# Performance work log

Measured on AMD Instinct MI355X. Metric: run time of the kernel, lower is better.

The kernel has to match this reference:

```python
import jax, jax.numpy as jnp
import numpy as np

N = 100000   # nodes in batched graph
E = 1600000  # edges (before self-loops)
D = 128      # in_dim == hidden_dim == num_outputs
G = 64       # graphs in the batch


def setup_inputs() -> dict:
    key = jax.random.key(0)
    ks = jax.random.split(key, 8)
    s = 1.0 / np.sqrt(D)
    x = jax.random.normal(ks[0], (N, D), jnp.float32)
    src = jax.random.randint(ks[1], (E,), 0, N, dtype=jnp.int64)
    dst = jax.random.randint(ks[2], (E,), 0, N, dtype=jnp.int64)
    graph_ids = jnp.sort(jax.random.randint(ks[3], (N,), 0, G, dtype=jnp.int64))
    W0 = jax.random.normal(ks[4], (D, D), jnp.float32) * s
    W1 = jax.random.normal(ks[5], (D, D), jnp.float32) * s
    W2 = jax.random.normal(ks[6], (D, D), jnp.float32) * s
    b0 = jnp.zeros((D,), jnp.float32)
    b1 = jnp.zeros((D,), jnp.float32)
    b2 = jnp.zeros((D,), jnp.float32)
    return {"x": x, "W0": W0, "b0": b0, "W1": W1, "b1": b1,
            "W2": W2, "b2": b2, "src": src, "dst": dst, "graph_ids": graph_ids}


def reference(x, W0, b0, W1, b1, W2, b2, src, dst, graph_ids):
    n = x.shape[0]
    loops = jnp.arange(n, dtype=src.dtype)
    src_f = jnp.concatenate([src, loops])  # add self-loops once (dgl.add_self_loop)
    dst_f = jnp.concatenate([dst, loops])
    ones_e = jnp.ones(src_f.shape, x.dtype)
    deg_out = jax.ops.segment_sum(ones_e, src_f, num_segments=n)  # >=1 (self-loop)
    deg_in = jax.ops.segment_sum(ones_e, dst_f, num_segments=n)
    cs = jax.lax.rsqrt(deg_out)[:, None]  # source norm (GraphConv norm='both')
    cd = jax.lax.rsqrt(deg_in)[:, None]   # destination norm

    def gcn_layer(h, W, b):
        m = (h * cs)[src_f]                                   # [E+N, D] gather
        agg = jax.ops.segment_sum(m, dst_f, num_segments=n)   # scatter-add SpMM
        return jax.nn.relu((agg * cd) @ W + b)                # F.relu(conv(g, h))

    h = gcn_layer(x, W0, b0)
    h = gcn_layer(h, W1, b1)
    h = gcn_layer(h, W2, b2)

    # dgl.mean_nodes: per-graph mean over nodes
    sums = jax.ops.segment_sum(h, graph_ids, num_segments=G)
    cnt = jax.ops.segment_sum(jnp.ones((n, 1), h.dtype), graph_ids, num_segments=G)
    return sums / jnp.maximum(cnt, 1.0)  # [G, D] logits
```

## Files before the change

### kernel.cpp

```cpp
#include <hip/hip_runtime.h>
#include <stdint.h>

#define D 128
#define CAP 64
#define HB 128
#define CH 25000

typedef __attribute__((ext_vector_type(8))) short bf16x8;
typedef __attribute__((ext_vector_type(4))) float f32x4;

__device__ inline unsigned short f2bf(float x) {
  union { float f; uint32_t u; } v; v.f = x;
  uint32_t u = v.u;
  u += 0x7fffu + ((u >> 16) & 1u);
  return (unsigned short)(u >> 16);
}
__device__ inline float bflo(uint32_t u) {
  union { uint32_t u; float f; } v; v.u = u << 16; return v.f;
}
__device__ inline float bfhi(uint32_t u) {
  union { uint32_t u; float f; } v; v.u = u & 0xffff0000u; return v.f;
}
__device__ inline uint32_t packbf(float lo, float hi) {
  return (uint32_t)f2bf(lo) | ((uint32_t)f2bf(hi) << 16);
}

__global__ __launch_bounds__(256) void hist_kernel(
    const int* __restrict__ src, const int* __restrict__ dst,
    unsigned int* __restrict__ parts_s, unsigned int* __restrict__ parts_d,
    int E, int N,
    const float* __restrict__ W0, const float* __restrict__ W1,
    const float* __restrict__ W2, unsigned short* __restrict__ Wt,
    int* __restrict__ cnt, int G, float* __restrict__ outz, int out_total) {
  __shared__ unsigned int lbs[CH / 8];
  __shared__ unsigned int lbd[CH / 8];
  int b = blockIdx.x & (HB - 1);
  int lo = (blockIdx.x >> 7) * CH;
  for (int i = threadIdx.x; i < CH / 8; i += 256) { lbs[i] = 0; lbd[i] = 0; }
  __syncthreads();
  int per = (E + HB - 1) / HB;
  int e0 = b * per;
  int e1 = min(e0 + per, E);
  for (int e = e0 + threadIdx.x; e < e1; e += 256) {
    int rs = src[e] - lo;
    if ((unsigned)rs < CH) atomicAdd(&lbs[rs >> 3], 1u << ((rs & 7) * 4));
    int rd = dst[e] - lo;
    if ((unsigned)rd < CH) atomicAdd(&lbd[rd >> 3], 1u << ((rd & 7) * 4));
  }
  __syncthreads();
  int nu = (N + 7) / 8;
  int base = lo >> 3;
  int cu = min(CH / 8, nu - base);
  unsigned int* ps = parts_s + (size_t)b * nu + base;
  unsigned int* pd = parts_d + (size_t)b * nu + base;
  for (int i = threadIdx.x; i < cu; i += 256) { ps[i] = lbs[i]; pd[i] = lbd[i]; }

  int gs = gridDim.x * 256;
  for (int i = blockIdx.x * 256 + threadIdx.x; i < 3 * 16384; i += gs) {
    int l = i >> 14, r = i & 16383;
    int n = r >> 7, k = r & 127;
    const float* W = (l == 0) ? W0 : (l == 1) ? W1 : W2;
    Wt[i] = f2bf(W[k * 128 + n]);
  }
  for (int i = blockIdx.x * 256 + threadIdx.x; i < G; i += gs) cnt[i] = 0;
  for (int i = blockIdx.x * 256 + threadIdx.x; i < out_total; i += gs) outz[i] = 0.f;
}

__global__ __launch_bounds__(256) void scan_norm_kernel(
    const unsigned char* __restrict__ parts_s,
    const unsigned char* __restrict__ parts_d,
    unsigned char* __restrict__ offs_d,
    int* __restrict__ degd,
    float* __restrict__ cs, float* __restrict__ cd,
    const int* __restrict__ gid, int* __restrict__ cnt,
    int N, int G) {
  __shared__ int lcnt[256];
  for (int i = threadIdx.x; i < G; i += 256) lcnt[i] = 0;
  __syncthreads();

  int t = blockIdx.x * blockDim.x + threadIdx.x;
  int i0 = t * 2;
  if (i0 < N) {
    int nb = N / 2;
    int ds0 = 0, ds1 = 0, dd0 = 0, dd1 = 0;
    for (int b = 0; b < HB; b++) {
      unsigned char sv = parts_s[(size_t)b * nb + t];
      ds0 += sv & 15; ds1 += sv >> 4;
      unsigned char dv = parts_d[(size_t)b * nb + t];
      offs_d[(size_t)b * N + i0]     = (unsigned char)min(dd0, 255);
      offs_d[(size_t)b * N + i0 + 1] = (unsigned char)min(dd1, 255);
      dd0 += dv & 15; dd1 += dv >> 4;
    }
    degd[i0] = dd0;     degd[i0 + 1] = dd1;
    cs[i0] = rsqrtf((float)ds0 + 1.0f);
    cs[i0 + 1] = rsqrtf((float)ds1 + 1.0f);
    cd[i0] = rsqrtf((float)dd0 + 1.0f);
    cd[i0 + 1] = rsqrtf((float)dd1 + 1.0f);
    atomicAdd(&lcnt[gid[i0]], 1);
    if (i0 + 1 < N) atomicAdd(&lcnt[gid[i0 + 1]], 1);
  }
  __syncthreads();
  for (int i = threadIdx.x; i < G; i += 256) {
    int c = lcnt[i];
    if (c) atomicAdd(&cnt[i], c);
  }
}

__global__ __launch_bounds__(256) void fill_kernel(
    const int* __restrict__ src, const int* __restrict__ dst,
    const unsigned char* __restrict__ offs_d, int* __restrict__ col, int E, int N,
    const float* __restrict__ x, const float* __restrict__ cs,
    uint32_t* __restrict__ xs) {
  __shared__ unsigned int lcur[CH / 8];
  int b = blockIdx.x & (HB - 1);
  int lo = (blockIdx.x >> 7) * CH;
  for (int i = threadIdx.x; i < CH / 8; i += 256) lcur[i] = 0;
  __syncthreads();
  int per = (E + HB - 1) / HB;
  int e0 = b * per;
  int e1 = min(e0 + per, E);
  const unsigned char* offb = offs_d + (size_t)b * N;
  for (int e = e0 + threadIdx.x; e < e1; e += 256) {
    int d = dst[e];
    int rd = d - lo;
    if ((unsigned)rd < CH) {
      unsigned old = atomicAdd(&lcur[rd >> 3], 1u << ((rd & 7) * 4));
      int local = (old >> ((rd & 7) * 4)) & 0xF;
      int pos = (int)offb[d] + local;
      if (pos < CAP) col[(size_t)d * CAP + pos] = src[e];
    }
  }
  int total2 = N * 64;
  int gs = gridDim.x * 256;
  for (int i = blockIdx.x * 256 + threadIdx.x; i < total2; i += gs) {
    float2 v = ((const float2*)x)[i];
    float c = cs[i >> 6];
    xs[i] = packbf(v.x * c, v.y * c);
  }
}

__global__ __launch_bounds__(512) void fused_layer_kernel(
    const uint32_t* __restrict__ hin, const unsigned short* __restrict__ Wt,
    const float* __restrict__ bias, const float* __restrict__ cd,
    const float* __restrict__ rowscale, const int* __restrict__ degd,
    const int* __restrict__ col, unsigned short* __restrict__ hout, int N) {
  __shared__ __align__(16) uint32_t At[16 * 68];

  int wv = threadIdx.x >> 6;
  int lane = threadIdx.x & 63;
  int m = lane & 15;
  int quad = lane >> 4;

  bf16x8 bfr[4];
#pragma unroll
  for (int c = 0; c < 4; c++)
    bfr[c] = *(const bf16x8*)(Wt + (size_t)(16 * wv + m) * 128 + c * 32 + quad * 8);

#pragma unroll
  for (int j = 0; j < 2; j++) {
    int w = __builtin_amdgcn_readfirstlane(blockIdx.x * 16 + wv * 2 + j);
    float accx = 0.f, accy = 0.f;
    if (w < N) {
      int n = min(degd[w], CAP);
      const int* cw = col + (size_t)w * CAP;
      const uint32_t* hl = hin + lane;
      uint32_t selfv = hl[(size_t)w * 64];
      accx = bflo(selfv); accy = bfhi(selfv);
      int i = 0;
      for (; i + 7 < n; i += 8) {
        int s0 = cw[i],     s1 = cw[i + 1], s2 = cw[i + 2], s3 = cw[i + 3];
        int s4 = cw[i + 4], s5 = cw[i + 5], s6 = cw[i + 6], s7 = cw[i + 7];
        uint32_t v0 = hl[(size_t)s0 * 64];
        uint32_t v1 = hl[(size_t)s1 * 64];
        uint32_t v2 = hl[(size_t)s2 * 64];
        uint32_t v3 = hl[(size_t)s3 * 64];
        uint32_t v4 = hl[(size_t)s4 * 64];
        uint32_t v5 = hl[(size_t)s5 * 64];
        uint32_t v6 = hl[(size_t)s6 * 64];
        uint32_t v7 = hl[(size_t)s7 * 64];
        accx += bflo(v0); accy += bfhi(v0);
        accx += bflo(v1); accy += bfhi(v1);
        accx += bflo(v2); accy += bfhi(v2);
        accx += bflo(v3); accy += bfhi(v3);
        accx += bflo(v4); accy += bfhi(v4);
        accx += bflo(v5); accy += bfhi(v5);
        accx += bflo(v6); accy += bfhi(v6);
        accx += bflo(v7); accy += bfhi(v7);
      }
      for (; i + 3 < n; i += 4) {
        int s0 = cw[i], s1 = cw[i + 1], s2 = cw[i + 2], s3 = cw[i + 3];
        uint32_t v0 = hl[(size_t)s0 * 64];
        uint32_t v1 = hl[(size_t)s1 * 64];
        uint32_t v2 = hl[(size_t)s2 * 64];
        uint32_t v3 = hl[(size_t)s3 * 64];
        accx += bflo(v0); accy += bfhi(v0);
        accx += bflo(v1); accy += bfhi(v1);
        accx += bflo(v2); accy += bfhi(v2);
        accx += bflo(v3); accy += bfhi(v3);
      }
      for (; i < n; i++) {
        uint32_t v = hl[(size_t)cw[i] * 64];
        accx += bflo(v); accy += bfhi(v);
      }
      float cdv = cd[w];
      accx *= cdv; accy *= cdv;
    }
    At[(wv * 2 + j) * 68 + lane] = packbf(accx, accy);
  }
  __syncthreads();

  const unsigned short* arow = (const unsigned short*)At + m * 136;
  f32x4 acc = f32x4{0.f, 0.f, 0.f, 0.f};
#pragma unroll
  for (int c = 0; c < 4; c++) {
    bf16x8 a = *(const bf16x8*)(arow + c * 32 + quad * 8);
    acc = __builtin_amdgcn_mfma_f32_16x16x32_bf16(a, bfr[c], acc, 0, 0, 0);
  }
  int colb = 16 * wv + m;
  float bv = bias[colb];
#pragma unroll
  for (int i = 0; i < 4; i++) {
    int r = blockIdx.x * 16 + quad * 4 + i;
    if (r < N) {
      float v = acc[i] + bv;
      v = v > 0.f ? v : 0.f;
      if (rowscale) v *= rowscale[r];
      hout[(size_t)r * D + colb] = f2bf(v);
    }
  }
}

__global__ void pool_kernel(const unsigned short* __restrict__ h, const int* __restrict__ gid,
                            float* __restrict__ outsum, const int* __restrict__ cnt, int N) {
  int v0 = blockIdx.x * 64;
  if (v0 >= N) return;
  int d = threadIdx.x;
  int vend = min(v0 + 64, N);
  int cur = gid[v0];
  float acc = 0.f;
  for (int v = v0; v < vend; v++) {
    int g = gid[v];
    if (g != cur) {
      float inv = 1.0f / fmaxf((float)cnt[cur], 1.0f);
      atomicAdd(&outsum[cur * D + d], acc * inv);
      acc = 0.f; cur = g;
    }
    unsigned short hv = __builtin_nontemporal_load(&h[(size_t)v * D + d]);
    union { uint32_t u; float f; } cv; cv.u = (uint32_t)hv << 16;
    acc += cv.f;
  }
  float inv = 1.0f / fmaxf((float)cnt[cur], 1.0f);
  atomicAdd(&outsum[cur * D + d], acc * inv);
}

extern "C" void kernel_launch(void* const* d_in, const int* in_sizes, int n_in,
                              void* d_out, int out_size, void* d_ws, size_t ws_size,
                              hipStream_t stream) {
  const float* x  = (const float*)d_in[0];
  const float* W0 = (const float*)d_in[1];
  const float* b0 = (const float*)d_in[2];
  const float* W1 = (const float*)d_in[3];
  const float* b1 = (const float*)d_in[4];
  const float* W2 = (const float*)d_in[5];
  const float* b2 = (const float*)d_in[6];
  const int* src  = (const int*)d_in[7];
  const int* dst  = (const int*)d_in[8];
  const int* gid  = (const int*)d_in[9];

  const int N = in_sizes[0] / D;
  const int E = in_sizes[7];
  const int G = out_size / D;
  const int nu = (N + 7) / 8;

  uint32_t* hsA = (uint32_t*)d_ws;
  uint32_t* hsB = hsA + (size_t)N * 64;
  int* col      = (int*)(hsB + (size_t)N * 64);
  int* degd     = col + (size_t)N * CAP;
  float* csb    = (float*)(degd + N);
  float* cdb    = csb + N;
  int* cnt      = (int*)(cdb + N);
  unsigned short* Wt = (unsigned short*)(cnt + G);
  unsigned int* parts_s = (unsigned int*)(Wt + 3 * 16384);
  unsigned int* parts_d = parts_s + (size_t)HB * nu;
  unsigned char* offs_d = (unsigned char*)(parts_d + (size_t)HB * nu);

  const int nch = (N + CH - 1) / CH;
  hist_kernel<<<HB * nch, 256, 0, stream>>>(src, dst, parts_s, parts_d, E, N,
                                            W0, W1, W2, Wt, cnt, G,
                                            (float*)d_out, out_size);
  scan_norm_kernel<<<(N / 2 + 255) / 256, 256, 0, stream>>>(
      (const unsigned char*)parts_s, (const unsigned char*)parts_d, offs_d,
      degd, csb, cdb, gid, cnt, N, G);
  fill_kernel<<<HB * nch, 256, 0, stream>>>(src, dst, offs_d, col, E, N, x, csb, hsA);

  const int ltiles = (N + 15) / 16;

  fused_layer_kernel<<<ltiles, 512, 0, stream>>>(hsA, Wt, b0, cdb, csb, degd, col,
                                                 (unsigned short*)hsB, N);
  fused_layer_kernel<<<ltiles, 512, 0, stream>>>(hsB, Wt + 16384, b1, cdb, csb, degd, col,
                                                 (unsigned short*)hsA, N);
  fused_layer_kernel<<<ltiles, 512, 0, stream>>>(hsA, Wt + 2 * 16384, b2, cdb, nullptr, degd, col,
                                                 (unsigned short*)hsB, N);

  pool_kernel<<<(N + 63) / 64, 128, 0, stream>>>((const unsigned short*)hsB, gid,
                                                 (float*)d_out, cnt, N);
}
```

Before: 454.1 us.

## Interleave two destination rows' gathers and broadcast neighbor indices via readlane

Each wave now loads its two destination rows' whole neighbor index lists with a single coalesced vector load (one index per lane) and pulls each source index out with readlane, instead of issuing scalar loads per neighbor. The gathers for both rows are interleaved in batches of eight so sixteen independent loads are in flight at once. Tail iterations are handled with masked eight-wide batches, and the launch bounds now request four blocks per SM. The aim is to raise memory-level parallelism in the latency-bound SpMM gather, at the cost of more registers and more complex control flow.

```diff
diff --git a/kernel.cpp b/kernel.cpp
--- a/kernel.cpp
+++ b/kernel.cpp
@@ -139,7 +139,7 @@
   }
 }
 
-__global__ __launch_bounds__(512) void fused_layer_kernel(
+__global__ __launch_bounds__(512, 4) void fused_layer_kernel(
     const uint32_t* __restrict__ hin, const unsigned short* __restrict__ Wt,
     const float* __restrict__ bias, const float* __restrict__ cd,
     const float* __restrict__ rowscale, const int* __restrict__ degd,
@@ -156,57 +156,94 @@
   for (int c = 0; c < 4; c++)
     bfr[c] = *(const bf16x8*)(Wt + (size_t)(16 * wv + m) * 128 + c * 32 + quad * 8);
 
-#pragma unroll
-  for (int j = 0; j < 2; j++) {
-    int w = __builtin_amdgcn_readfirstlane(blockIdx.x * 16 + wv * 2 + j);
-    float accx = 0.f, accy = 0.f;
-    if (w < N) {
-      int n = min(degd[w], CAP);
-      const int* cw = col + (size_t)w * CAP;
-      const uint32_t* hl = hin + lane;
-      uint32_t selfv = hl[(size_t)w * 64];
-      accx = bflo(selfv); accy = bfhi(selfv);
-      int i = 0;
-      for (; i + 7 < n; i += 8) {
-        int s0 = cw[i],     s1 = cw[i + 1], s2 = cw[i + 2], s3 = cw[i + 3];
-        int s4 = cw[i + 4], s5 = cw[i + 5], s6 = cw[i + 6], s7 = cw[i + 7];
-        uint32_t v0 = hl[(size_t)s0 * 64];
-        uint32_t v1 = hl[(size_t)s1 * 64];
-        uint32_t v2 = hl[(size_t)s2 * 64];
-        uint32_t v3 = hl[(size_t)s3 * 64];
-        uint32_t v4 = hl[(size_t)s4 * 64];
-        uint32_t v5 = hl[(size_t)s5 * 64];
-        uint32_t v6 = hl[(size_t)s6 * 64];
-        uint32_t v7 = hl[(size_t)s7 * 64];
-        accx += bflo(v0); accy += bfhi(v0);
-        accx += bflo(v1); accy += bfhi(v1);
-        accx += bflo(v2); accy += bfhi(v2);
-        accx += bflo(v3); accy += bfhi(v3);
-        accx += bflo(v4); accy += bfhi(v4);
-        accx += bflo(v5); accy += bfhi(v5);
-        accx += bflo(v6); accy += bfhi(v6);
-        accx += bflo(v7); accy += bfhi(v7);
-      }
-      for (; i + 3 < n; i += 4) {
-        int s0 = cw[i], s1 = cw[i + 1], s2 = cw[i + 2], s3 = cw[i + 3];
-        uint32_t v0 = hl[(size_t)s0 * 64];
-        uint32_t v1 = hl[(size_t)s1 * 64];
-        uint32_t v2 = hl[(size_t)s2 * 64];
-        uint32_t v3 = hl[(size_t)s3 * 64];
-        accx += bflo(v0); accy += bfhi(v0);
-        accx += bflo(v1); accy += bfhi(v1);
-        accx += bflo(v2); accy += bfhi(v2);
-        accx += bflo(v3); accy += bfhi(v3);
-      }
-      for (; i < n; i++) {
-        uint32_t v = hl[(size_t)cw[i] * 64];
-        accx += bflo(v); accy += bfhi(v);
-      }
-      float cdv = cd[w];
-      accx *= cdv; accy *= cdv;
-    }
-    At[(wv * 2 + j) * 68 + lane] = packbf(accx, accy);
-  }
+  int w0 = blockIdx.x * 16 + wv * 2;
+  int w1 = w0 + 1;
+  float ax0 = 0.f, ay0 = 0.f, ax1 = 0.f, ay1 = 0.f;
+  int n0 = 0, n1 = 0;
+  int idx0 = 0, idx1 = 0;
+  if (w0 < N) {
+    n0 = min(degd[w0], CAP);
+    idx0 = col[(size_t)w0 * CAP + lane];
+    uint32_t sv = hin[(size_t)w0 * 64 + lane];
+    ax0 = bflo(sv); ay0 = bfhi(sv);
+  }
+  if (w1 < N) {
+    n1 = min(degd[w1], CAP);
+    idx1 = col[(size_t)w1 * CAP + lane];
+    uint32_t sv = hin[(size_t)w1 * 64 + lane];
+    ax1 = bflo(sv); ay1 = bfhi(sv);
+  }
+  const uint32_t* hl = hin + lane;
+  int i0 = 0, i1 = 0;
+  while (i0 + 8 <= n0 && i1 + 8 <= n1) {
+    uint32_t v0[8], v1[8];
+#pragma unroll
+    for (int k = 0; k < 8; k++) {
+      int s = __builtin_amdgcn_readlane(idx0, i0 + k);
+      v0[k] = hl[(size_t)s * 64];
+    }
+#pragma unroll
+    for (int k = 0; k < 8; k++) {
+      int s = __builtin_amdgcn_readlane(idx1, i1 + k);
+      v1[k] = hl[(size_t)s * 64];
+    }
+#pragma unroll
+    for (int k = 0; k < 8; k++) { ax0 += bflo(v0[k]); ay0 += bfhi(v0[k]); }
+#pragma unroll
+    for (int k = 0; k < 8; k++) { ax1 += bflo(v1[k]); ay1 += bfhi(v1[k]); }
+    i0 += 8; i1 += 8;
+  }
+  while (i0 + 8 <= n0) {
+    uint32_t v[8];
+#pragma unroll
+    for (int k = 0; k < 8; k++) {
+      int s = __builtin_amdgcn_readlane(idx0, i0 + k);
+      v[k] = hl[(size_t)s * 64];
+    }
+#pragma unroll
+    for (int k = 0; k < 8; k++) { ax0 += bflo(v[k]); ay0 += bfhi(v[k]); }
+    i0 += 8;
+  }
+  if (i0 < n0) {
+    uint32_t v[8];
+#pragma unroll
+    for (int k = 0; k < 8; k++) {
+      if (i0 + k < n0) {
+        int s = __builtin_amdgcn_readlane(idx0, i0 + k);
+        v[k] = hl[(size_t)s * 64];
+      } else v[k] = 0;
+    }
+#pragma unroll
+    for (int k = 0; k < 8; k++) { ax0 += bflo(v[k]); ay0 += bfhi(v[k]); }
+  }
+  while (i1 + 8 <= n1) {
+    uint32_t v[8];
+#pragma unroll
+    for (int k = 0; k < 8; k++) {
+      int s = __builtin_amdgcn_readlane(idx1, i1 + k);
+      v[k] = hl[(size_t)s * 64];
+    }
+#pragma unroll
+    for (int k = 0; k < 8; k++) { ax1 += bflo(v[k]); ay1 += bfhi(v[k]); }
+    i1 += 8;
+  }
+  if (i1 < n1) {
+    uint32_t v[8];
+#pragma unroll
+    for (int k = 0; k < 8; k++) {
+      if (i1 + k < n1) {
+        int s = __builtin_amdgcn_readlane(idx1, i1 + k);
+        v[k] = hl[(size_t)s * 64];
+      } else v[k] = 0;
+    }
+#pragma unroll
+    for (int k = 0; k < 8; k++) { ax1 += bflo(v[k]); ay1 += bfhi(v[k]); }
+  }
+
+  if (w0 < N) { float c = cd[w0]; ax0 *= c; ay0 *= c; }
+  if (w1 < N) { float c = cd[w1]; ax1 *= c; ay1 *= c; }
+  At[(wv * 2 + 0) * 68 + lane] = packbf(ax0, ay0);
+  At[(wv * 2 + 1) * 68 + lane] = packbf(ax1, ay1);
   __syncthreads();
 
   const unsigned short* arow = (const unsigned short*)At + m * 136;
```

Measured after the change: 481.1 us. 5.9% more time.
